# Optimization experiments

Hardware: AMD Instinct MI355X
Metric: run time of the kernel (lower is better)

## Reference

```python
import jax, jax.numpy as jnp
from jax import lax
import numpy as np

ITER_ = 10
SMOOTH = 1.0

# ---------- soft skeletonization (clDice-style, 2D) ----------

def _max_pool(x, wh, ww):
    # x: [B,1,H,W]
    return lax.reduce_window(x, -jnp.inf, lax.max, (1, 1, wh, ww), (1, 1, 1, 1), 'SAME')

def _soft_erode(x):
    return jnp.minimum(-_max_pool(-x, 3, 1), -_max_pool(-x, 1, 3))

def _soft_dilate(x):
    return _max_pool(x, 3, 3)

def _soft_open(x):
    return _soft_dilate(_soft_erode(x))

def soft_skel(img, iters):
    skel = jax.nn.relu(img - _soft_open(img))
    for _ in range(iters):
        img = _soft_erode(img)
        delta = jax.nn.relu(img - _soft_open(img))
        skel = skel + jax.nn.relu(delta - skel * delta)
    return skel

# ---------- exact 2D Euclidean distance transform ----------

def _edt2d(mask):
    # mask: [H,W] bool, True = foreground. distance to nearest background pixel.
    H, W = mask.shape
    BIG = jnp.float32(H + W)
    z = ~mask  # background indicator
    def step(d, zr):
        d = jnp.where(zr, 0.0, jnp.minimum(d + 1.0, BIG))
        return d, d
    init = jnp.full((H,), BIG, jnp.float32)
    _, f = lax.scan(step, init, z.T)            # [W,H] forward along rows
    _, b = lax.scan(step, init, z.T[::-1])      # backward
    g = jnp.minimum(f, b[::-1]).T               # [H,W] 1D row distance
    ys = jnp.arange(H, dtype=jnp.float32)
    diff2 = (ys[:, None] - ys[None, :]) ** 2    # [H,H]
    # lower envelope over columns: d2[y,x] = min_y' g[y',x]^2 + (y-y')^2
    d2 = jnp.min(g[None, :, :] ** 2 + diff2[:, :, None], axis=1)  # [H,W]
    return jnp.sqrt(d2)

_edt_batched = jax.vmap(_edt2d)  # [B,H,W] bool -> [B,H,W] float

# ---------- cbDice pieces ----------

def combine_tensors(A, B, C):
    return jnp.where((A != 0) & (B == 0), A * C, B * C)

def get_weights(mask_input, skel_input, prob_flag):
    # mask_input/skel_input: [B,H,W] float
    mask = mask_input > 0.5
    skel = skel_input > 0.5
    dist = lax.stop_gradient(_edt_batched(mask))       # EDT of binary mask, non-diff
    distances = jnp.where(mask, dist, 0.0)
    skel_radius = jnp.where(skel, distances, 0.0)
    rmax = jnp.maximum(jnp.max(skel_radius, axis=(1, 2), keepdims=True), 1.0)
    rmin = jnp.maximum(jnp.min(skel_radius, axis=(1, 2), keepdims=True), 1.0)
    d_clip = jnp.minimum(distances, rmax)
    dist_map_norm = d_clip / rmax
    skel_R_norm = skel_radius / rmax
    I_norm = (rmax - skel_radius + rmin) / rmax        # dim == 2 branch
    I_norm = jnp.where(skel, I_norm, 0.0)
    if prob_flag:
        return dist_map_norm * mask_input, skel_R_norm * mask_input, I_norm * skel_input
    m = mask.astype(jnp.float32)
    s = skel.astype(jnp.float32)
    return dist_map_norm * m, skel_R_norm * m, I_norm * s

def soft_cb_dice_loss(y_pred, y_true):
    p = jax.nn.sigmoid(y_pred)                              # [B,1,H,W]
    pb = jnp.concatenate([1.0 - p, p], axis=1)              # [B,2,H,W]
    pp = jax.nn.softmax(pb, axis=1)[:, 1]                   # [B,H,W]
    yt = jnp.where(y_true > 0, 1.0, 0.0)[:, 0]              # [B,H,W]
    hard = lax.stop_gradient((pp > 0.5).astype(jnp.float32))
    skel_pred_hard = lax.stop_gradient(soft_skel(hard[:, None], ITER_)[:, 0])
    skel_true = lax.stop_gradient(soft_skel(yt[:, None], ITER_)[:, 0])
    skel_pred_prob = skel_pred_hard * pp
    q_vl, q_slvl, q_sl = get_weights(yt, skel_true, False)
    q_vp, q_spvp, q_sp = get_weights(pp, skel_pred_prob, True)
    w_tprec = (jnp.sum(q_sp * q_vl) + SMOOTH) / (jnp.sum(combine_tensors(q_spvp, q_slvl, q_sp)) + SMOOTH)
    w_tsens = (jnp.sum(q_sl * q_vp) + SMOOTH) / (jnp.sum(combine_tensors(q_slvl, q_spvp, q_sl)) + SMOOTH)
    return 1.0 - 2.0 * (w_tprec * w_tsens) / (w_tprec + w_tsens)

def setup_inputs() -> dict:
    key = jax.random.key(0)
    k1, k2 = jax.random.split(key)
    y_pred = jax.random.normal(k1, (4, 1, 256, 256), dtype=jnp.float32)
    y_true = jax.random.randint(k2, (4, 1, 256, 256), 0, 2, dtype=jnp.int32)
    return {"y_pred": y_pred, "y_true": y_true}

def reference(y_pred, y_true):
    return soft_cb_dice_loss(y_pred, y_true)
```

## Files before the change

### kernel.cpp

```cpp
#include <hip/hip_runtime.h>

typedef unsigned long long u64;

#define NIMG 4
#define H 256
#define W 256
#define NPIX (H*W)
#define NTOT (NIMG*NPIX)
#define WPR 4
#define WPI (H*WPR)
#define WPB (NIMG*WPI)
#define XT 8
#define NSKEL 8
#define NTILE 128
#define NB2 (NSKEL+NTILE)

__device__ __forceinline__ void erode_from(const u64 S[][WPR], int y, u64 out[WPR]) {
  u64 c[WPR], up[WPR], dn[WPR];
#pragma unroll
  for (int k = 0; k < WPR; ++k) {
    c[k]  = S[y][k];
    up[k] = (y > 0)     ? S[y-1][k] : ~0ULL;
    dn[k] = (y < H-1)   ? S[y+1][k] : ~0ULL;
  }
#pragma unroll
  for (int k = 0; k < WPR; ++k) {
    u64 l = (c[k] << 1) | ((k > 0)     ? (c[k-1] >> 63) : 1ULL);
    u64 r = (c[k] >> 1) | ((k < WPR-1) ? (c[k+1] << 63) : 0x8000000000000000ULL);
    out[k] = c[k] & up[k] & dn[k] & l & r;
  }
}

__device__ __forceinline__ void dilate_from(const u64 S[][WPR], int y, u64 out[WPR]) {
  u64 v[WPR];
#pragma unroll
  for (int k = 0; k < WPR; ++k) {
    u64 a = S[y][k];
    if (y > 0)   a |= S[y-1][k];
    if (y < H-1) a |= S[y+1][k];
    v[k] = a;
  }
#pragma unroll
  for (int k = 0; k < WPR; ++k) {
    u64 l = (v[k] << 1) | ((k > 0)     ? (v[k-1] >> 63) : 0ULL);
    u64 r = (v[k] >> 1) | ((k < WPR-1) ? (v[k+1] << 63) : 0ULL);
    out[k] = v[k] | l | r;
  }
}

__global__ void __launch_bounds__(256) prep_kernel(
    const float* __restrict__ y_pred, const int* __restrict__ y_true,
    u64* __restrict__ mask_bits, unsigned* __restrict__ rmm_u,
    double* __restrict__ sums, unsigned* __restrict__ cnts) {
  if (blockIdx.x == 0) {
    if (threadIdx.x < 16) rmm_u[threadIdx.x] = (threadIdx.x & 1) ? 0x7F800000u : 0u;
    else if (threadIdx.x < 20) sums[threadIdx.x - 16] = 0.0;
    else if (threadIdx.x < 34) cnts[threadIdx.x - 20] = 0u;
  }
  int i = blockIdx.x * 256 + threadIdx.x;
  float x = y_pred[i];
  float p = 1.0f / (1.0f + expf(-x));
  float q = 1.0f / (1.0f + expf(-(2.0f * p - 1.0f)));
  u64 bt = __ballot(y_true[i] > 0);
  u64 bp = __ballot(q > 0.5f);
  if ((threadIdx.x & 63) == 0) {
    mask_bits[i >> 6] = bt;
    mask_bits[WPB + (i >> 6)] = bp;
  }
}

#define EDT_PASS(MROW, DIST, SAVE_MASK)                                        \
  {                                                                            \
    int y = t;                                                                 \
    const u64* row = (MROW) + y*WPR;                                           \
    u64 z[WPR];                                                                \
    _Pragma("unroll")                                                          \
    for (int k = 0; k < WPR; ++k) z[k] = ~row[k];         \
    if (SAVE_MASK) msk_row[y] = row[kx];                                       \
    _Pragma("unroll")                                                          \
    for (int xx = 0; xx < XT; ++xx) {                                          \
      int x = x0 + xx;                                                         \
      int bx = x & 63;                                                         \
      int ld = 512;                                                            \
      {                                                                        \
        u64 w = z[kx] & ((bx == 63) ? ~0ULL : ((1ULL << (bx+1)) - 1ULL));      \
        for (int k = kx; ; ) {                                                 \
          if (w) { int pos = 63 - __builtin_clzll(w) + (k << 6); ld = x - pos; break; } \
          if (--k < 0) break;                                                  \
          w = z[k];                                                            \
        }                                                                      \
      }                                                                        \
      int rd = 512;                                                            \
      {                                                                        \
        u64 w = z[kx] & (~0ULL << bx);                                         \
        for (int k = kx; ; ) {                                                 \
          if (w) { int pos = __builtin_ctzll(w) + (k << 6); rd = pos - x; break; } \
          if (++k > WPR-1) break;                                              \
          w = z[k];                                                            \
        }                                                                      \
      }                                                                        \
      int g = min(ld, rd);                                                     \
      col2[y][xx] = (float)(g * g);                                            \
    }                                                                          \
  }                                                                            \
  __syncthreads();                                                             \
  _Pragma("unroll")                                                            \
  for (int j = 0; j < 8; ++j) {                                                \
    int y = yg * 8 + j;                                                        \
    float best = col2[y][xq];                                                  \
    for (int k = 1; k < H; ++k) {                                              \
      float k2 = (float)(k * k);                                               \
      if (k2 >= best) break;                \
      int ym = y - k, yd = y + k;                                              \
      if (ym >= 0) best = fminf(best, col2[ym][xq] + k2);                      \
      if (yd < H)  best = fminf(best, col2[yd][xq] + k2);                      \
    }                                                                          \
    (DIST)[j] = sqrtf(best);                                                   \
  }                                                                            \
  __syncthreads();

__global__ void __launch_bounds__(256, 1) fused_kernel(
    const float* __restrict__ y_pred, const u64* __restrict__ mask_bits,
    u64* __restrict__ skel_bits, unsigned* __restrict__ rmm_u,
    double* __restrict__ sums, unsigned* __restrict__ cnts,
    float* __restrict__ out) {
  __shared__ u64 SA[H][WPR];
  __shared__ u64 SB[H][WPR];
  __shared__ float col2[H][XT + 1];
  __shared__ u64 srow_t[H];
  __shared__ u64 srow_p[H];
  __shared__ u64 msk_row[H];
  __shared__ float redf[4][4];
  __shared__ unsigned smm[4];
  int t = threadIdx.x;

  if (blockIdx.x < NSKEL) {
    int bi = blockIdx.x;
    int y = t;
    int base = bi * WPI;
    u64 a[WPR], cur[WPR], e[WPR], d[WPR], sk[WPR];
#pragma unroll
    for (int k = 0; k < WPR; ++k) { a[k] = mask_bits[base + y*WPR + k]; SA[y][k] = a[k]; }
    __syncthreads();
    erode_from(SA, y, e);
#pragma unroll
    for (int k = 0; k < WPR; ++k) SB[y][k] = e[k];
    __syncthreads();
    dilate_from(SB, y, d);
#pragma unroll
    for (int k = 0; k < WPR; ++k) { sk[k] = a[k] & ~d[k]; cur[k] = e[k]; }
    u64 (*P)[WPR] = SB;
    u64 (*Q)[WPR] = SA;
    for (int it = 0; it < 10; ++it) {
      erode_from(P, y, e);
#pragma unroll
      for (int k = 0; k < WPR; ++k) Q[y][k] = e[k];
      __syncthreads();
      dilate_from(Q, y, d);
#pragma unroll
      for (int k = 0; k < WPR; ++k) { sk[k] |= cur[k] & ~d[k]; cur[k] = e[k]; }
      u64 (*T)[WPR] = P; P = Q; Q = T;
    }
#pragma unroll
    for (int k = 0; k < WPR; ++k) skel_bits[base + y*WPR + k] = sk[k];
    __syncthreads();
    if (t == 0) {
      __threadfence();
      atomicAdd(&cnts[bi], 1u);
    }
    return;
  }

  int tb  = blockIdx.x - NSKEL;
  int img = tb >> 5;
  int xt  = tb & 31;
  int x0  = xt * XT;
  int kx  = x0 >> 6;
  int sh0 = x0 & 63;
  int xq  = t & (XT - 1);
  int yg  = t >> 3;

  float dist_t[8], dist_p[8];
  EDT_PASS(mask_bits + img*WPI,       dist_t, 1)
  EDT_PASS(mask_bits + (4+img)*WPI,   dist_p, 0)

  if (t == 0) {
    while (__hip_atomic_load(&cnts[img], __ATOMIC_RELAXED,
                             __HIP_MEMORY_SCOPE_AGENT) == 0u)
      __builtin_amdgcn_s_sleep(2);
    while (__hip_atomic_load(&cnts[4+img], __ATOMIC_RELAXED,
                             __HIP_MEMORY_SCOPE_AGENT) == 0u)
      __builtin_amdgcn_s_sleep(2);
  }
  __syncthreads();
  srow_t[t] = __hip_atomic_load(&skel_bits[img*WPI + t*WPR + kx],
                                __ATOMIC_RELAXED, __HIP_MEMORY_SCOPE_AGENT);
  srow_p[t] = __hip_atomic_load(&skel_bits[(4+img)*WPI + t*WPR + kx],
                                __ATOMIC_RELAXED, __HIP_MEMORY_SCOPE_AGENT);
  __syncthreads();

  float vmax_t = 0.0f, vmin_t = 3.0e38f, vmax_p = 0.0f, vmin_p = 3.0e38f;
#pragma unroll
  for (int j = 0; j < 8; ++j) {
    int y = yg * 8 + j;
    int sb_t = (int)((srow_t[y] >> (sh0 + xq)) & 1ULL);
    int sb_p = (int)((srow_p[y] >> (sh0 + xq)) & 1ULL);
    float srt = sb_t ? dist_t[j] : 0.0f;
    float srp = sb_p ? dist_p[j] : 0.0f;
    vmax_t = fmaxf(vmax_t, srt); vmin_t = fminf(vmin_t, srt);
    vmax_p = fmaxf(vmax_p, srp); vmin_p = fminf(vmin_p, srp);
  }
  for (int o = 32; o > 0; o >>= 1) {
    vmax_t = fmaxf(vmax_t, __shfl_down(vmax_t, o, 64));
    vmin_t = fminf(vmin_t, __shfl_down(vmin_t, o, 64));
    vmax_p = fmaxf(vmax_p, __shfl_down(vmax_p, o, 64));
    vmin_p = fminf(vmin_p, __shfl_down(vmin_p, o, 64));
  }
  int wave = t >> 6, lane = t & 63;
  if (lane == 0) { redf[wave][0]=vmax_t; redf[wave][1]=vmin_t;
                   redf[wave][2]=vmax_p; redf[wave][3]=vmin_p; }
  __syncthreads();
  if (t == 0) {
    float mxt=redf[0][0], mnt=redf[0][1], mxp=redf[0][2], mnp=redf[0][3];
    for (int wv = 1; wv < 4; ++wv) {
      mxt = fmaxf(mxt, redf[wv][0]); mnt = fminf(mnt, redf[wv][1]);
      mxp = fmaxf(mxp, redf[wv][2]); mnp = fminf(mnp, redf[wv][3]);
    }
    atomicMax(&rmm_u[img*2 + 0], __float_as_uint(mxt));
    atomicMin(&rmm_u[img*2 + 1], __float_as_uint(mnt));
    atomicMax(&rmm_u[(4+img)*2 + 0], __float_as_uint(mxp));
    atomicMin(&rmm_u[(4+img)*2 + 1], __float_as_uint(mnp));
    __hip_atomic_fetch_add(&cnts[10+img], 1u, __ATOMIC_RELEASE,
                           __HIP_MEMORY_SCOPE_AGENT);
    while (__hip_atomic_load(&cnts[10+img], __ATOMIC_RELAXED,
                             __HIP_MEMORY_SCOPE_AGENT) < 32u)
      __builtin_amdgcn_s_sleep(2);
  }
  __syncthreads();
  if (t < 4) {
    int idx = (t < 2) ? (img*2 + t) : ((4+img)*2 + (t-2));
    smm[t] = __hip_atomic_load(&rmm_u[idx], __ATOMIC_RELAXED,
                               __HIP_MEMORY_SCOPE_AGENT);
  }
  __syncthreads();
  float rmax_t = fmaxf(__uint_as_float(smm[0]), 1.0f);
  float rmin_t = fmaxf(__uint_as_float(smm[1]), 1.0f);
  float rmax_p = fmaxf(__uint_as_float(smm[2]), 1.0f);
  float rmin_p = fmaxf(__uint_as_float(smm[3]), 1.0f);

  float q1 = 0.f, q2 = 0.f, q3 = 0.f, q4 = 0.f;
#pragma unroll
  for (int j = 0; j < 8; ++j) {
    int y = yg * 8 + j;
    float xv = y_pred[img*NPIX + y*W + x0 + xq];
    float p = 1.0f / (1.0f + expf(-xv));
    float ppv = 1.0f / (1.0f + expf(-(2.0f * p - 1.0f)));
    int b = sh0 + xq;
    int m_t  = (int)((msk_row[y] >> b) & 1ULL);
    int s_t  = (int)((srow_t[y] >> b) & 1ULL);
    int s_pb = (int)((srow_p[y] >> b) & 1ULL);
    float distances_t = m_t ? dist_t[j] : 0.0f;
    float skelrad_t   = s_t ? distances_t : 0.0f;
    float dmn_t = fminf(distances_t, rmax_t) / rmax_t;
    float srn_t = skelrad_t / rmax_t;
    float In_t  = s_t ? (rmax_t - skelrad_t + rmin_t) / rmax_t : 0.0f;
    float q_vl   = m_t ? dmn_t : 0.0f;
    float q_slvl = m_t ? srn_t : 0.0f;
    float q_sl   = s_t ? In_t  : 0.0f;
    float skel_in_p = s_pb ? ppv : 0.0f;
    bool msk_p = ppv > 0.5f;
    bool sk_p  = skel_in_p > 0.5f;
    float distances_p = msk_p ? dist_p[j] : 0.0f;
    float skelrad_p   = sk_p ? distances_p : 0.0f;
    float dmn_p = fminf(distances_p, rmax_p) / rmax_p;
    float srn_p = skelrad_p / rmax_p;
    float In_p  = sk_p ? (rmax_p - skelrad_p + rmin_p) / rmax_p : 0.0f;
    float q_vp   = dmn_p * ppv;
    float q_spvp = srn_p * ppv;
    float q_sp   = In_p * skel_in_p;
    q1 += q_sp * q_vl;
    q2 += (q_spvp != 0.0f && q_slvl == 0.0f) ? q_spvp * q_sp : q_slvl * q_sp;
    q3 += q_sl * q_vp;
    q4 += (q_slvl != 0.0f && q_spvp == 0.0f) ? q_slvl * q_sl : q_spvp * q_sl;
  }
  for (int o = 32; o > 0; o >>= 1) {
    q1 += __shfl_down(q1, o, 64);
    q2 += __shfl_down(q2, o, 64);
    q3 += __shfl_down(q3, o, 64);
    q4 += __shfl_down(q4, o, 64);
  }
  if (lane == 0) { redf[wave][0]=q1; redf[wave][1]=q2; redf[wave][2]=q3; redf[wave][3]=q4; }
  __syncthreads();
  if (t == 0) {
    float a0=0,a1=0,a2=0,a3=0;
    for (int wv = 0; wv < 4; ++wv) {
      a0 += redf[wv][0]; a1 += redf[wv][1]; a2 += redf[wv][2]; a3 += redf[wv][3];
    }
    atomicAdd(&sums[0], (double)a0);
    atomicAdd(&sums[1], (double)a1);
    atomicAdd(&sums[2], (double)a2);
    atomicAdd(&sums[3], (double)a3);
    __threadfence();
    unsigned c = atomicAdd(&cnts[8], 1u);
    if (c == NTILE - 1) {
      double s0 = atomicAdd(&sums[0], 0.0);
      double s1 = atomicAdd(&sums[1], 0.0);
      double s2 = atomicAdd(&sums[2], 0.0);
      double s3 = atomicAdd(&sums[3], 0.0);
      double wp  = (s0 + 1.0) / (s1 + 1.0);
      double wsn = (s2 + 1.0) / (s3 + 1.0);
      out[0] = (float)(1.0 - 2.0 * (wp * wsn) / (wp + wsn));
    }
  }
}

extern "C" void kernel_launch(void* const* d_in, const int* in_sizes, int n_in,
                              void* d_out, int out_size, void* d_ws, size_t ws_size,
                              hipStream_t stream) {
  (void)in_sizes; (void)n_in; (void)out_size; (void)ws_size;
  const float* y_pred = (const float*)d_in[0];
  const int*   y_true = (const int*)d_in[1];
  float* out = (float*)d_out;
  char* ws = (char*)d_ws;

  u64*   mask_bits = (u64*)  (ws + 0);
  u64*   skel_bits = (u64*)  (ws + 65536);
  unsigned* rmm_u  = (unsigned*)(ws + 131072);
  double* sums     = (double*)(ws + 131136);
  unsigned* cnts   = (unsigned*)(ws + 131168);

  prep_kernel<<<NTOT/256, 256, 0, stream>>>(y_pred, y_true, mask_bits, rmm_u, sums, cnts);
  fused_kernel<<<NB2, 256, 0, stream>>>(y_pred, mask_bits, skel_bits, rmm_u, sums, cnts, out);
}
```

Before: 90.99 us.

## Fuse mask bit-packing into main kernel and replace prep kernel with memset

Removes the separate prep kernel. Each skeleton block and EDT tile block now builds the packed mask rows directly from y_true and y_pred with vectorized loads into shared memory, and the pred mask is taken as y_pred > 0 instead of recomputing the sigmoids. Workspace counters are zeroed with hipMemsetAsync, and the min reduction is recast as an atomicMax on the bitwise complement so zero-init works. This saves a launch and the global round-trip for mask bits, but each EDT tile block now re-reads a full image of both inputs, which means redundant global traffic.

After: 101.8 us. 1.12x slower.

```diff
diff --git a/kernel.cpp b/kernel.cpp
--- a/kernel.cpp
+++ b/kernel.cpp
@@ -9,11 +9,10 @@
 #define NTOT (NIMG*NPIX)
 #define WPR 4
 #define WPI (H*WPR)
-#define WPB (NIMG*WPI)
 #define XT 8
 #define NSKEL 8
 #define NTILE 128
-#define NB2 (NSKEL+NTILE)
+#define NB (NSKEL+NTILE)
 
 __device__ __forceinline__ void erode_from(const u64 S[][WPR], int y, u64 out[WPR]) {
   u64 c[WPR], up[WPR], dn[WPR];
@@ -48,35 +47,46 @@
   }
 }
 
-__global__ void __launch_bounds__(256) prep_kernel(
-    const float* __restrict__ y_pred, const int* __restrict__ y_true,
-    u64* __restrict__ mask_bits, unsigned* __restrict__ rmm_u,
-    double* __restrict__ sums, unsigned* __restrict__ cnts) {
-  if (blockIdx.x == 0) {
-    if (threadIdx.x < 16) rmm_u[threadIdx.x] = (threadIdx.x & 1) ? 0x7F800000u : 0u;
-    else if (threadIdx.x < 20) sums[threadIdx.x - 16] = 0.0;
-    else if (threadIdx.x < 34) cnts[threadIdx.x - 20] = 0u;
-  }
-  int i = blockIdx.x * 256 + threadIdx.x;
-  float x = y_pred[i];
-  float p = 1.0f / (1.0f + expf(-x));
-  float q = 1.0f / (1.0f + expf(-(2.0f * p - 1.0f)));
-  u64 bt = __ballot(y_true[i] > 0);
-  u64 bp = __ballot(q > 0.5f);
-  if ((threadIdx.x & 63) == 0) {
-    mask_bits[i >> 6] = bt;
-    mask_bits[WPB + (i >> 6)] = bp;
-  }
-}
-
-#define EDT_PASS(MROW, DIST, SAVE_MASK)                                        \
+__device__ __forceinline__ void build_row_true(const int* __restrict__ img_base,
+                                               int y, u64 out[WPR]) {
+  const int4* s = (const int4*)(img_base + y * W);
+#pragma unroll
+  for (int k = 0; k < WPR; ++k) {
+    u64 w = 0;
+#pragma unroll
+    for (int m = 0; m < 16; ++m) {
+      int4 v = s[k*16 + m];
+      unsigned nib = (unsigned)(v.x > 0) | ((unsigned)(v.y > 0) << 1)
+                   | ((unsigned)(v.z > 0) << 2) | ((unsigned)(v.w > 0) << 3);
+      w |= (u64)nib << (4*m);
+    }
+    out[k] = w;
+  }
+}
+
+__device__ __forceinline__ void build_row_pred(const float* __restrict__ img_base,
+                                               int y, u64 out[WPR]) {
+  const float4* s = (const float4*)(img_base + y * W);
+#pragma unroll
+  for (int k = 0; k < WPR; ++k) {
+    u64 w = 0;
+#pragma unroll
+    for (int m = 0; m < 16; ++m) {
+      float4 v = s[k*16 + m];
+      unsigned nib = (unsigned)(v.x > 0.0f) | ((unsigned)(v.y > 0.0f) << 1)
+                   | ((unsigned)(v.z > 0.0f) << 2) | ((unsigned)(v.w > 0.0f) << 3);
+      w |= (u64)nib << (4*m);
+    }
+    out[k] = w;
+  }
+}
+
+#define EDT_PASS(MARR, DIST)                                                   \
   {                                                                            \
     int y = t;                                                                 \
-    const u64* row = (MROW) + y*WPR;                                           \
     u64 z[WPR];                                                                \
     _Pragma("unroll")                                                          \
-    for (int k = 0; k < WPR; ++k) z[k] = ~row[k];         \
-    if (SAVE_MASK) msk_row[y] = row[kx];                                       \
+    for (int k = 0; k < WPR; ++k) z[k] = ~MARR[y][k];     \
     _Pragma("unroll")                                                          \
     for (int xx = 0; xx < XT; ++xx) {                                          \
       int x = x0 + xx;                                                         \
@@ -120,7 +130,7 @@
   __syncthreads();
 
 __global__ void __launch_bounds__(256, 1) fused_kernel(
-    const float* __restrict__ y_pred, const u64* __restrict__ mask_bits,
+    const float* __restrict__ y_pred, const int* __restrict__ y_true,
     u64* __restrict__ skel_bits, unsigned* __restrict__ rmm_u,
     double* __restrict__ sums, unsigned* __restrict__ cnts,
     float* __restrict__ out) {
@@ -129,18 +139,19 @@
   __shared__ float col2[H][XT + 1];
   __shared__ u64 srow_t[H];
   __shared__ u64 srow_p[H];
-  __shared__ u64 msk_row[H];
   __shared__ float redf[4][4];
   __shared__ unsigned smm[4];
   int t = threadIdx.x;
 
   if (blockIdx.x < NSKEL) {
-    int bi = blockIdx.x;
+    int bi  = blockIdx.x;
+    int img = bi & 3;
     int y = t;
-    int base = bi * WPI;
     u64 a[WPR], cur[WPR], e[WPR], d[WPR], sk[WPR];
-#pragma unroll
-    for (int k = 0; k < WPR; ++k) { a[k] = mask_bits[base + y*WPR + k]; SA[y][k] = a[k]; }
+    if (bi < 4) build_row_true(y_true + img*NPIX, y, a);
+    else        build_row_pred(y_pred + img*NPIX, y, a);
+#pragma unroll
+    for (int k = 0; k < WPR; ++k) SA[y][k] = a[k];
     __syncthreads();
     erode_from(SA, y, e);
 #pragma unroll
@@ -161,6 +172,7 @@
       for (int k = 0; k < WPR; ++k) { sk[k] |= cur[k] & ~d[k]; cur[k] = e[k]; }
       u64 (*T)[WPR] = P; P = Q; Q = T;
     }
+    int base = bi * WPI;
 #pragma unroll
     for (int k = 0; k < WPR; ++k) skel_bits[base + y*WPR + k] = sk[k];
     __syncthreads();
@@ -180,9 +192,18 @@
   int xq  = t & (XT - 1);
   int yg  = t >> 3;
 
+  {
+    u64 rt[WPR], rp[WPR];
+    build_row_true(y_true + img*NPIX, t, rt);
+    build_row_pred(y_pred + img*NPIX, t, rp);
+#pragma unroll
+    for (int k = 0; k < WPR; ++k) { SA[t][k] = rt[k]; SB[t][k] = rp[k]; }
+  }
+  __syncthreads();
+
   float dist_t[8], dist_p[8];
-  EDT_PASS(mask_bits + img*WPI,       dist_t, 1)
-  EDT_PASS(mask_bits + (4+img)*WPI,   dist_p, 0)
+  EDT_PASS(SA, dist_t)
+  EDT_PASS(SB, dist_p)
 
   if (t == 0) {
     while (__hip_atomic_load(&cnts[img], __ATOMIC_RELAXED,
@@ -226,10 +247,10 @@
       mxt = fmaxf(mxt, redf[wv][0]); mnt = fminf(mnt, redf[wv][1]);
       mxp = fmaxf(mxp, redf[wv][2]); mnp = fminf(mnp, redf[wv][3]);
     }
-    atomicMax(&rmm_u[img*2 + 0], __float_as_uint(mxt));
-    atomicMin(&rmm_u[img*2 + 1], __float_as_uint(mnt));
+    atomicMax(&rmm_u[img*2 + 0],     __float_as_uint(mxt));
+    atomicMax(&rmm_u[img*2 + 1],     ~__float_as_uint(mnt));
     atomicMax(&rmm_u[(4+img)*2 + 0], __float_as_uint(mxp));
-    atomicMin(&rmm_u[(4+img)*2 + 1], __float_as_uint(mnp));
+    atomicMax(&rmm_u[(4+img)*2 + 1], ~__float_as_uint(mnp));
     __hip_atomic_fetch_add(&cnts[10+img], 1u, __ATOMIC_RELEASE,
                            __HIP_MEMORY_SCOPE_AGENT);
     while (__hip_atomic_load(&cnts[10+img], __ATOMIC_RELAXED,
@@ -243,10 +264,10 @@
                                __HIP_MEMORY_SCOPE_AGENT);
   }
   __syncthreads();
-  float rmax_t = fmaxf(__uint_as_float(smm[0]), 1.0f);
-  float rmin_t = fmaxf(__uint_as_float(smm[1]), 1.0f);
-  float rmax_p = fmaxf(__uint_as_float(smm[2]), 1.0f);
-  float rmin_p = fmaxf(__uint_as_float(smm[3]), 1.0f);
+  float rmax_t = fmaxf(__uint_as_float( smm[0]), 1.0f);
+  float rmin_t = fmaxf(__uint_as_float(~smm[1]), 1.0f);
+  float rmax_p = fmaxf(__uint_as_float( smm[2]), 1.0f);
+  float rmin_p = fmaxf(__uint_as_float(~smm[3]), 1.0f);
 
   float q1 = 0.f, q2 = 0.f, q3 = 0.f, q4 = 0.f;
 #pragma unroll
@@ -256,7 +277,7 @@
     float p = 1.0f / (1.0f + expf(-xv));
     float ppv = 1.0f / (1.0f + expf(-(2.0f * p - 1.0f)));
     int b = sh0 + xq;
-    int m_t  = (int)((msk_row[y] >> b) & 1ULL);
+    int m_t  = (int)((SA[y][kx] >> b) & 1ULL);
     int s_t  = (int)((srow_t[y] >> b) & 1ULL);
     int s_pb = (int)((srow_p[y] >> b) & 1ULL);
     float distances_t = m_t ? dist_t[j] : 0.0f;
@@ -323,12 +344,11 @@
   float* out = (float*)d_out;
   char* ws = (char*)d_ws;
 
-  u64*   mask_bits = (u64*)  (ws + 0);
-  u64*   skel_bits = (u64*)  (ws + 65536);
-  unsigned* rmm_u  = (unsigned*)(ws + 131072);
-  double* sums     = (double*)(ws + 131136);
-  unsigned* cnts   = (unsigned*)(ws + 131168);
-
-  prep_kernel<<<NTOT/256, 256, 0, stream>>>(y_pred, y_true, mask_bits, rmm_u, sums, cnts);
-  fused_kernel<<<NB2, 256, 0, stream>>>(y_pred, mask_bits, skel_bits, rmm_u, sums, cnts, out);
-}
+  u64*   skel_bits = (u64*)  (ws + 0);
+  unsigned* rmm_u  = (unsigned*)(ws + 65536);
+  double* sums     = (double*)(ws + 65600);
+  unsigned* cnts   = (unsigned*)(ws + 65632);
+
+  hipMemsetAsync(ws + 65536, 0, 160, stream);
+  fused_kernel<<<NB, 256, 0, stream>>>(y_pred, y_true, skel_bits, rmm_u, sums, cnts, out);
+}
```
